# Performance work log

Hardware: AMD Instinct MI355X
Metric: run time of the kernel (lower is better)

## Reference

```python
import jax, jax.numpy as jnp
import numpy as np

T, H = 2048, 2048          # tokens, hidden_size
E, I = 16, 768             # num_experts, moe_intermediate_size
K = 2                      # top_k


def setup_inputs() -> dict:
    key = jax.random.key(0)
    k1, k2, k3, k4, k5 = jax.random.split(key, 5)
    hidden_states = jax.random.normal(k1, (T, H), dtype=jnp.float32)
    top_k_index = jax.random.randint(k2, (T, K), 0, E, dtype=jnp.int64)
    top_k_weights = jax.random.uniform(k3, (T, K), dtype=jnp.float32)
    gate_up_proj = jax.random.normal(k4, (E, 2 * I, H), dtype=jnp.float32) * 0.02
    down_proj = jax.random.normal(k5, (E, H, I), dtype=jnp.float32) * 0.02
    return {
        "hidden_states": hidden_states,
        "top_k_index": top_k_index,
        "top_k_weights": top_k_weights,
        "gate_up_proj": gate_up_proj,
        "down_proj": down_proj,
    }


def reference(hidden_states, top_k_index, top_k_weights, gate_up_proj, down_proj):
    # Dense combine-weight matrix C[t, e] = sum of routing weights of token t for expert e.
    # Scatter-add matches index_add_ semantics (duplicate expert picks sum their weights,
    # which equals the eager per-(token, k) accumulation since the expert FFN is the same).
    t_idx = jnp.arange(hidden_states.shape[0])[:, None]
    C = jnp.zeros((hidden_states.shape[0], gate_up_proj.shape[0]), dtype=hidden_states.dtype)
    C = C.at[t_idx, top_k_index].add(top_k_weights.astype(hidden_states.dtype))

    inter = down_proj.shape[2]
    # [T, E, 2I]: each expert's gate_up GEMM applied to every token (zero-weight tokens
    # contribute nothing after combining with C).
    gu = jnp.einsum("th,eoh->teo", hidden_states, gate_up_proj)
    gate, up = gu[..., :inter], gu[..., inter:]
    h = jax.nn.silu(gate) * up                      # [T, E, I]
    y = jnp.einsum("tei,ehi->teh", h, down_proj)    # [T, E, H]
    return jnp.einsum("teh,te->th", y, C)           # weighted combine -> [T, H]
```

## Files before the change

kernel.cpp:

```cpp
#include <hip/hip_runtime.h>
#include <hip/hip_bf16.h>
#include <cstdint>
#include <cstddef>

#define T_TOK 2048
#define HID   2048
#define NEXP  16
#define INTER 768
#define TOPK  2
#define CAP   1024
#define MBLK  8

using short8  = __attribute__((ext_vector_type(8))) short;
using f32x16  = __attribute__((ext_vector_type(16))) float;

#define MFMA(a,b,c) __builtin_amdgcn_mfma_f32_32x32x16_bf16((a),(b),(c),0,0,0)

__device__ inline ushort bf16h(float x) {
    union { __hip_bfloat16 b; ushort u; } cv; cv.b = __float2bfloat16(x); return cv.u;
}
__device__ inline void gl16(const void* g, void* l) {
    __builtin_amdgcn_global_load_lds((const __attribute__((address_space(1))) void*)g,
                                     (__attribute__((address_space(3))) void*)l, 16, 0, 0);
}
__device__ inline void split8(float4 a, float4 b, short8& h, short8& l) {
    float v[8] = {a.x,a.y,a.z,a.w,b.x,b.y,b.z,b.w};
    #pragma unroll
    for (int j = 0; j < 8; ++j) {
        ushort hb = bf16h(v[j]);
        float hf = __uint_as_float(((uint32_t)hb) << 16);
        h[j] = (short)hb;
        l[j] = (short)bf16h(v[j] - hf);
    }
}

__global__ __launch_bounds__(256)
void route_kernel(const int* __restrict__ idx, const float* __restrict__ wts,
                  int* __restrict__ counts, int* __restrict__ pair_tk,
                  float* __restrict__ pair_w) {
    int p = blockIdx.x * blockDim.x + threadIdx.x;
    if (p >= T_TOK * TOPK) return;
    int e = idx[p];
    int pos = atomicAdd(&counts[e], 1);
    if (pos < CAP) {
        pair_tk[e * CAP + pos] = p;
        pair_w [e * CAP + pos] = wts[p];
    }
}

__global__ __launch_bounds__(256)
void prep_bf16_kernel(const float4* __restrict__ src, ushort4* __restrict__ dst, int n4) {
    int stride = gridDim.x * blockDim.x;
    for (int i = blockIdx.x*blockDim.x + threadIdx.x; i < n4; i += stride) {
        float4 v = src[i];
        dst[i] = make_ushort4(bf16h(v.x), bf16h(v.y), bf16h(v.z), bf16h(v.w));
    }
}

__global__ __launch_bounds__(256)
void prep_hilo_kernel(const float4* __restrict__ src, ushort4* __restrict__ hi,
                      ushort4* __restrict__ lo, int n4) {
    int stride = gridDim.x * blockDim.x;
    for (int i = blockIdx.x*blockDim.x + threadIdx.x; i < n4; i += stride) {
        float4 v = src[i];
        ushort h0=bf16h(v.x), h1=bf16h(v.y), h2=bf16h(v.z), h3=bf16h(v.w);
        hi[i] = make_ushort4(h0,h1,h2,h3);
        lo[i] = make_ushort4(bf16h(v.x - __uint_as_float((uint32_t)h0<<16)),
                             bf16h(v.y - __uint_as_float((uint32_t)h1<<16)),
                             bf16h(v.z - __uint_as_float((uint32_t)h2<<16)),
                             bf16h(v.w - __uint_as_float((uint32_t)h3<<16)));
    }
}

__global__ __launch_bounds__(256, 3)
void s1mm_kernel(const ushort* __restrict__ hshi, const ushort* __restrict__ hslo,
                 const ushort* __restrict__ gupb,
                 const int* __restrict__ counts, const int* __restrict__ pair_tk,
                 float* __restrict__ gu) {
    __shared__ ushort Ab[2][8*512];
    __shared__ ushort Bb[2][16*512];
    __shared__ int s_tk[64];

    const int lin  = blockIdx.x;
    const int work = (lin & 7)*192 + (lin >> 3);
    const int x = work % 6, y = (work/6) & 7, z = work/48;
    const int e = z >> 1, ks = z & 1;
    const int cnt = min(counts[e], CAP);
    const int m0 = y*64;
    if (m0 >= cnt) return;
    const int n0 = x*128;

    const int tid = threadIdx.x, ln = tid & 63, w = tid >> 6;
    if (tid < 64) s_tk[tid] = pair_tk[e*CAP + min(m0+tid, cnt-1)];
    __syncthreads();

    const int lr = ln & 31, oc = (ln >> 5)*8;
    const int tkA = s_tk[(w & 1)*32 + lr];
    const ushort* hp = (w >> 1) ? hslo : hshi;
    const ushort* aA = hp + (size_t)(tkA >> 1)*HID + ks*1024 + oc;
    const ushort* bG = gupb + ((size_t)e*(2*INTER) + (n0 + w*32 + lr))*HID + ks*1024 + oc;
    const ushort* bU = gupb + ((size_t)e*(2*INTER) + (INTER + n0 + w*32 + lr))*HID + ks*1024 + oc;

    f32x16 accg[2], accu[2];
    #pragma unroll
    for (int i=0;i<16;++i){accg[0][i]=0.f;accg[1][i]=0.f;accu[0][i]=0.f;accu[1][i]=0.f;}

#define S1_STAGE(buf, k32) { const int kb=(k32)*32;            \
    gl16(aA+kb,    &Ab[buf][(2*w+0)*512]);                     \
    gl16(aA+kb+16, &Ab[buf][(2*w+1)*512]);                     \
    gl16(bG+kb,    &Bb[buf][(2*w+0)*512]);                     \
    gl16(bG+kb+16, &Bb[buf][(2*w+1)*512]);                     \
    gl16(bU+kb,    &Bb[buf][(2*(4+w)+0)*512]);                 \
    gl16(bU+kb+16, &Bb[buf][(2*(4+w)+1)*512]); }

    S1_STAGE(0, 0)
    int cur = 0;
    const int ro = ln*8;
    for (int k32 = 0; k32 < 32; ++k32) {
        __syncthreads();
        if (k32 + 1 < 32) S1_STAGE(cur^1, k32+1)
        #pragma unroll
        for (int kf = 0; kf < 2; ++kf) {
            short8 ah0 = *(const short8*)&Ab[cur][(0+kf)*512 + ro];
            short8 ah1 = *(const short8*)&Ab[cur][(2+kf)*512 + ro];
            short8 al0 = *(const short8*)&Ab[cur][(4+kf)*512 + ro];
            short8 al1 = *(const short8*)&Ab[cur][(6+kf)*512 + ro];
            short8 bg  = *(const short8*)&Bb[cur][(2*w+kf)*512 + ro];
            short8 bu  = *(const short8*)&Bb[cur][(8+2*w+kf)*512 + ro];
            accg[0]=MFMA(ah0,bg,accg[0]); accg[0]=MFMA(al0,bg,accg[0]);
            accg[1]=MFMA(ah1,bg,accg[1]); accg[1]=MFMA(al1,bg,accg[1]);
            accu[0]=MFMA(ah0,bu,accu[0]); accu[0]=MFMA(al0,bu,accu[0]);
            accu[1]=MFMA(ah1,bu,accu[1]); accu[1]=MFMA(al1,bu,accu[1]);
        }
        cur ^= 1;
    }
#undef S1_STAGE

    const int crhi = (ln>>5)*4, cl = ln&31;
    const int colg = n0 + 32*w + cl;
    #pragma unroll
    for (int mi=0;mi<2;++mi)
      #pragma unroll
      for (int r=0;r<16;++r) {
        int row = mi*32 + (r&3) + 8*(r>>2) + crhi;
        if (m0 + row < cnt) {
            size_t base = (size_t)s_tk[row]*(2*INTER);
            atomicAdd(&gu[base + colg],         accg[mi][r]);
            atomicAdd(&gu[base + INTER + colg], accu[mi][r]);
        }
      }
}

__global__ __launch_bounds__(256)
void fuse_kernel(const float* __restrict__ gu, ushort* __restrict__ hhi,
                 ushort* __restrict__ hlo) {
    int id  = blockIdx.x*256 + threadIdx.x;
    int row = id / (INTER/4);
    int c4  = (id % (INTER/4)) * 4;
    const float* gr = gu + (size_t)row*(2*INTER) + c4;
    float4 g = *(const float4*)gr;
    float4 u = *(const float4*)(gr + INTER);
    float hv[4];
    hv[0] = g.x/(1.f+__expf(-g.x))*u.x;
    hv[1] = g.y/(1.f+__expf(-g.y))*u.y;
    hv[2] = g.z/(1.f+__expf(-g.z))*u.z;
    hv[3] = g.w/(1.f+__expf(-g.w))*u.w;
    ushort h0=bf16h(hv[0]), h1=bf16h(hv[1]), h2=bf16h(hv[2]), h3=bf16h(hv[3]);
    *(ushort4*)&hhi[(size_t)row*INTER + c4] = make_ushort4(h0,h1,h2,h3);
    *(ushort4*)&hlo[(size_t)row*INTER + c4] = make_ushort4(
        bf16h(hv[0]-__uint_as_float((uint32_t)h0<<16)),
        bf16h(hv[1]-__uint_as_float((uint32_t)h1<<16)),
        bf16h(hv[2]-__uint_as_float((uint32_t)h2<<16)),
        bf16h(hv[3]-__uint_as_float((uint32_t)h3<<16)));
}

__global__ __launch_bounds__(256, 3)
void s2mm_kernel(const ushort* __restrict__ h2hi, const ushort* __restrict__ h2lo,
                 const ushort* __restrict__ dwnb,
                 const int* __restrict__ counts, const int* __restrict__ pair_tk,
                 const float* __restrict__ pair_w, float* __restrict__ out) {
    __shared__ ushort Ab[2][8*512];
    __shared__ ushort Bb[2][16*512];
    __shared__ int   s_tk[64];
    __shared__ float s_w[64];

    const int lin  = blockIdx.x;
    const int work = (lin & 7)*256 + (lin >> 3);
    const int x = work & 7, y = (work >> 3) & 7, z = work >> 6;
    const int e = z >> 1, ks = z & 1;
    const int cnt = min(counts[e], CAP);
    const int m0 = y*64;
    if (m0 >= cnt) return;
    const int n0 = x*256;

    const int tid = threadIdx.x, ln = tid & 63, w = tid >> 6;
    if (tid < 64) {
        int s = min(m0+tid, cnt-1);
        s_tk[tid] = pair_tk[e*CAP + s];
        s_w[tid]  = pair_w [e*CAP + s];
    }
    __syncthreads();

    const int lr = ln & 31, oc = (ln >> 5)*8;
    const int tkA = s_tk[(w & 1)*32 + lr];
    const ushort* hp = (w >> 1) ? h2lo : h2hi;
    const ushort* aA = hp + (size_t)tkA*INTER + ks*384 + oc;
    const ushort* b0 = dwnb + ((size_t)e*HID + (n0 + (2*w+0)*32 + lr))*INTER + ks*384 + oc;
    const ushort* b1 = dwnb + ((size_t)e*HID + (n0 + (2*w+1)*32 + lr))*INTER + ks*384 + oc;

    f32x16 acc[2][2];
    #pragma unroll
    for (int mi=0;mi<2;++mi)
      #pragma unroll
      for (int ni=0;ni<2;++ni)
        #pragma unroll
        for (int i=0;i<16;++i) acc[mi][ni][i] = 0.f;

#define S2_STAGE(buf, k32) { const int kb=(k32)*32;            \
    gl16(aA+kb,    &Ab[buf][(2*w+0)*512]);                     \
    gl16(aA+kb+16, &Ab[buf][(2*w+1)*512]);                     \
    gl16(b0+kb,    &Bb[buf][(4*w+0)*512]);                     \
    gl16(b0+kb+16, &Bb[buf][(4*w+1)*512]);                     \
    gl16(b1+kb,    &Bb[buf][(4*w+2)*512]);                     \
    gl16(b1+kb+16, &Bb[buf][(4*w+3)*512]); }

    S2_STAGE(0, 0)
    int cur = 0;
    const int ro = ln*8;
    for (int k32 = 0; k32 < 12; ++k32) {
        __syncthreads();
        if (k32 + 1 < 12) S2_STAGE(cur^1, k32+1)
        #pragma unroll
        for (int kf = 0; kf < 2; ++kf) {
            short8 ah0 = *(const short8*)&Ab[cur][(0+kf)*512 + ro];
            short8 ah1 = *(const short8*)&Ab[cur][(2+kf)*512 + ro];
            short8 al0 = *(const short8*)&Ab[cur][(4+kf)*512 + ro];
            short8 al1 = *(const short8*)&Ab[cur][(6+kf)*512 + ro];
            short8 b0f = *(const short8*)&Bb[cur][(4*w+0+kf)*512 + ro];
            short8 b1f = *(const short8*)&Bb[cur][(4*w+2+kf)*512 + ro];
            acc[0][0]=MFMA(ah0,b0f,acc[0][0]); acc[0][0]=MFMA(al0,b0f,acc[0][0]);
            acc[1][0]=MFMA(ah1,b0f,acc[1][0]); acc[1][0]=MFMA(al1,b0f,acc[1][0]);
            acc[0][1]=MFMA(ah0,b1f,acc[0][1]); acc[0][1]=MFMA(al0,b1f,acc[0][1]);
            acc[1][1]=MFMA(ah1,b1f,acc[1][1]); acc[1][1]=MFMA(al1,b1f,acc[1][1]);
        }
        cur ^= 1;
    }
#undef S2_STAGE

    const int crhi = (ln>>5)*4, cl = ln&31;
    #pragma unroll
    for (int mi=0;mi<2;++mi)
      #pragma unroll
      for (int r=0;r<16;++r) {
        int row = mi*32 + (r&3) + 8*(r>>2) + crhi;
        if (m0 + row < cnt) {
            int   t  = s_tk[row] >> 1;
            float wt = s_w[row];
            #pragma unroll
            for (int ni=0;ni<2;++ni) {
                int col = n0 + 64*w + 32*ni + cl;
                atomicAdd(&out[(size_t)t*HID + col], wt*acc[mi][ni][r]);
            }
        }
      }
}

__global__ __launch_bounds__(256)
void s1_fb_kernel(const float* __restrict__ hs, const float* __restrict__ gup,
                  const int* __restrict__ counts, const int* __restrict__ pair_tk,
                  float* __restrict__ gu) {
    __shared__ ushort Ahi[4*512], Alo[4*512];
    __shared__ ushort Bhi[16*512], Blo[16*512];
    __shared__ int s_tk[64];
    const int e  = blockIdx.z >> 1;
    const int ks = blockIdx.z & 1;
    const int cnt = min(counts[e], CAP);
    const int m0  = blockIdx.y * 64;
    if (m0 >= cnt) return;
    const int n0  = blockIdx.x * 128;
    const int tid = threadIdx.x, lane = tid & 63, w = tid >> 6;
    if (tid < 64) s_tk[tid] = pair_tk[e*CAP + min(m0+tid, cnt-1)];
    __syncthreads();
    const int ar = tid & 63, aq = tid >> 6;
    const float* asrc = hs + (size_t)(s_tk[ar] >> 1)*HID + ks*1024 + aq*8;
    const int br = tid;
    const float* bsrc = gup + (size_t)e*(2*INTER)*HID
                      + (size_t)((br < 128) ? (n0+br) : (INTER + n0 + br - 128))*HID + ks*1024;
    const int fA  = (ar>>5)*2 + (aq>>1);
    const int lnA = (ar&31) + 32*(aq&1);
    const int rgB = br >> 5, lnB = br & 31;
    f32x16 accg[2], accu[2];
    #pragma unroll
    for (int i=0;i<16;++i){ accg[0][i]=0.f; accg[1][i]=0.f; accu[0][i]=0.f; accu[1][i]=0.f; }
    float4 a0c,a1c,bvc[8], a0n,a1n,bvn[8];
    a0c = *(const float4*)(asrc + 0);
    a1c = *(const float4*)(asrc + 4);
    #pragma unroll
    for (int q=0;q<8;++q) bvc[q] = *(const float4*)(bsrc + 4*q);
#define S1_BODY(A0,A1,BV,A0N,A1N,BVN,KST)                                        \
    {                                                                            \
        __syncthreads();                                                         \
        { short8 h,l; split8(A0,A1,h,l);                                         \
          *(short8*)&Ahi[(fA<<9)+(lnA<<3)] = h;                                  \
          *(short8*)&Alo[(fA<<9)+(lnA<<3)] = l; }                                \
        _Pragma("unroll")                                                        \
        for (int o=0;o<4;++o) { short8 h,l; split8(BV[2*o],BV[2*o+1],h,l);       \
          int f = rgB*2 + (o>>1); int ln2 = lnB + 32*(o&1);                      \
          *(short8*)&Bhi[(f<<9)+(ln2<<3)] = h;                                   \
          *(short8*)&Blo[(f<<9)+(ln2<<3)] = l; }                                 \
        if ((KST)+1 < 32) {                                                     \
            int ko = ((KST)+1)*32;                                              \
            A0N = *(const float4*)(asrc + ko);                                  \
            A1N = *(const float4*)(asrc + ko + 4);                              \
            _Pragma("unroll")                                                   \
            for (int q=0;q<8;++q) BVN[q] = *(const float4*)(bsrc + ko + 4*q);   \
        }                                                                       \
        __syncthreads();                                                        \
        const int ro = lane << 3;                                               \
        _Pragma("unroll")                                                       \
        for (int kf=0;kf<2;++kf) {                                              \
            short8 ah0 = *(const short8*)&Ahi[((0*2+kf)<<9)+ro];                \
            short8 ah1 = *(const short8*)&Ahi[((1*2+kf)<<9)+ro];                \
            short8 al0 = *(const short8*)&Alo[((0*2+kf)<<9)+ro];                \
            short8 al1 = *(const short8*)&Alo[((1*2+kf)<<9)+ro];                \
            short8 bgh = *(const short8*)&Bhi[(((w  )*2+kf)<<9)+ro];            \
            short8 bgl = *(const short8*)&Blo[(((w  )*2+kf)<<9)+ro];            \
            short8 buh = *(const short8*)&Bhi[(((4+w)*2+kf)<<9)+ro];            \
            short8 bul = *(const short8*)&Blo[(((4+w)*2+kf)<<9)+ro];            \
            accg[0] = MFMA(ah0,bgh,accg[0]);                                    \
            accg[1] = MFMA(ah1,bgh,accg[1]);                                    \
            accu[0] = MFMA(ah0,buh,accu[0]);                                    \
            accu[1] = MFMA(ah1,buh,accu[1]);                                    \
            accg[0] = MFMA(al0,bgh,accg[0]);                                    \
            accg[1] = MFMA(al1,bgh,accg[1]);                                    \
            accu[0] = MFMA(al0,buh,accu[0]);                                    \
            accu[1] = MFMA(al1,buh,accu[1]);                                    \
            accg[0] = MFMA(ah0,bgl,accg[0]);                                    \
            accg[1] = MFMA(ah1,bgl,accg[1]);                                    \
            accu[0] = MFMA(ah0,bul,accu[0]);                                    \
            accu[1] = MFMA(ah1,bul,accu[1]);                                    \
        }                                                                       \
    }
    for (int kst = 0; kst < 32; kst += 2) {
        S1_BODY(a0c,a1c,bvc,a0n,a1n,bvn,kst)
        S1_BODY(a0n,a1n,bvn,a0c,a1c,bvc,kst+1)
    }
#undef S1_BODY
    const int crhi = (lane>>5)*4, cl = lane&31;
    const int colg = n0 + 32*w + cl;
    #pragma unroll
    for (int mi=0;mi<2;++mi)
      #pragma unroll
      for (int r=0;r<16;++r) {
        int row = mi*32 + (r&3) + 8*(r>>2) + crhi;
        if (m0 + row < cnt) {
            size_t base = (size_t)s_tk[row]*(2*INTER);
            atomicAdd(&gu[base + colg],         accg[mi][r]);
            atomicAdd(&gu[base + INTER + colg], accu[mi][r]);
        }
      }
}

__global__ __launch_bounds__(256)
void s2_fb_kernel(const ushort* __restrict__ hhi, const ushort* __restrict__ hlo,
                  const float* __restrict__ dwn, const int* __restrict__ counts,
                  const int* __restrict__ pair_tk, const float* __restrict__ pair_w,
                  float* __restrict__ out) {
    __shared__ ushort Ahi[4*512], Alo[4*512];
    __shared__ ushort Bhi[16*512], Blo[16*512];
    __shared__ int   s_tk[64];
    __shared__ float s_w[64];
    const int e  = blockIdx.z >> 1;
    const int ks = blockIdx.z & 1;
    const int cnt = min(counts[e], CAP);
    const int m0  = blockIdx.y * 64;
    if (m0 >= cnt) return;
    const int n0  = blockIdx.x * 256;
    const int tid = threadIdx.x, lane = tid & 63, w = tid >> 6;
    if (tid < 64) {
        int slot = min(m0+tid, cnt-1);
        s_tk[tid] = pair_tk[e*CAP + slot];
        s_w[tid]  = pair_w [e*CAP + slot];
    }
    __syncthreads();
    const int fA = tid >> 6, lnA = tid & 63;
    const int arow = (fA>>1)*32 + (lnA & 31);
    const int aoct = lnA >> 5, akf = fA & 1;
    const size_t aoff = (size_t)s_tk[arow]*INTER + ks*384 + akf*16 + aoct*8;
    const ushort* ahsrc = hhi + aoff;
    const ushort* alsrc = hlo + aoff;
    const int br = tid;
    const float* bsrc = dwn + (size_t)e*HID*INTER + (size_t)(n0+br)*INTER + ks*384;
    const int rgB = br >> 5, lnB = br & 31;
    f32x16 acc[2][2];
    #pragma unroll
    for (int mi=0;mi<2;++mi)
      #pragma unroll
      for (int ni=0;ni<2;++ni)
        #pragma unroll
        for (int i=0;i<16;++i) acc[mi][ni][i] = 0.f;
    short8 ahc, alc, ahn, aln;
    float4 bvc[8], bvn[8];
    ahc = *(const short8*)(ahsrc);
    alc = *(const short8*)(alsrc);
    #pragma unroll
    for (int q=0;q<8;++q) bvc[q] = *(const float4*)(bsrc + 4*q);
#define S2_BODY(AH,AL,BV,AHN,ALN,BVN,KST)                                        \
    {                                                                            \
        __syncthreads();                                                         \
        *(short8*)&Ahi[(fA<<9)+(lnA<<3)] = AH;                                   \
        *(short8*)&Alo[(fA<<9)+(lnA<<3)] = AL;                                   \
        _Pragma("unroll")                                                        \
        for (int o=0;o<4;++o) { short8 h,l; split8(BV[2*o],BV[2*o+1],h,l);       \
          int f = rgB*2 + (o>>1); int ln2 = lnB + 32*(o&1);                      \
          *(short8*)&Bhi[(f<<9)+(ln2<<3)] = h;                                   \
          *(short8*)&Blo[(f<<9)+(ln2<<3)] = l; }                                 \
        if ((KST)+1 < 12) {                                                     \
            int ko = ((KST)+1)*32;                                              \
            AHN = *(const short8*)(ahsrc + ko);                                 \
            ALN = *(const short8*)(alsrc + ko);                                 \
            _Pragma("unroll")                                                   \
            for (int q=0;q<8;++q) BVN[q] = *(const float4*)(bsrc + ko + 4*q);   \
        }                                                                       \
        __syncthreads();                                                        \
        const int ro = lane << 3;                                               \
        _Pragma("unroll")                                                       \
        for (int kf=0;kf<2;++kf) {                                              \
            short8 ah0 = *(const short8*)&Ahi[((0*2+kf)<<9)+ro];                \
            short8 ah1 = *(const short8*)&Ahi[((1*2+kf)<<9)+ro];                \
            short8 al0 = *(const short8*)&Alo[((0*2+kf)<<9)+ro];                \
            short8 al1 = *(const short8*)&Alo[((1*2+kf)<<9)+ro];                \
            _Pragma("unroll")                                                   \
            for (int ni=0;ni<2;++ni) {                                          \
                short8 bh = *(const short8*)&Bhi[(((2*w+ni)*2+kf)<<9)+ro];      \
                short8 bl = *(const short8*)&Blo[(((2*w+ni)*2+kf)<<9)+ro];      \
                acc[0][ni] = MFMA(ah0,bh,acc[0][ni]);                           \
                acc[1][ni] = MFMA(ah1,bh,acc[1][ni]);                           \
                acc[0][ni] = MFMA(al0,bh,acc[0][ni]);                           \
                acc[1][ni] = MFMA(al1,bh,acc[1][ni]);                           \
                acc[0][ni] = MFMA(ah0,bl,acc[0][ni]);                           \
                acc[1][ni] = MFMA(ah1,bl,acc[1][ni]);                           \
            }                                                                   \
        }                                                                       \
    }
    for (int kst = 0; kst < 12; kst += 2) {
        S2_BODY(ahc,alc,bvc,ahn,aln,bvn,kst)
        S2_BODY(ahn,aln,bvn,ahc,alc,bvc,kst+1)
    }
#undef S2_BODY
    const int crhi = (lane>>5)*4, cl = lane&31;
    #pragma unroll
    for (int mi=0;mi<2;++mi)
      #pragma unroll
      for (int r=0;r<16;++r) {
        int row = mi*32 + (r&3) + 8*(r>>2) + crhi;
        if (m0 + row < cnt) {
            int   t  = s_tk[row] >> 1;
            float wt = s_w[row];
            #pragma unroll
            for (int ni=0;ni<2;++ni) {
                int col = n0 + 64*w + 32*ni + cl;
                atomicAdd(&out[(size_t)t*HID + col], wt*acc[mi][ni][r]);
            }
        }
      }
}

extern "C" void kernel_launch(void* const* d_in, const int* in_sizes, int n_in,
                              void* d_out, int out_size, void* d_ws, size_t ws_size,
                              hipStream_t stream) {
    const float* hs  = (const float*)d_in[0];
    const int*   idx = (const int*)  d_in[1];
    const float* wts = (const float*)d_in[2];
    const float* gup = (const float*)d_in[3];
    const float* dwn = (const float*)d_in[4];
    float* out = (float*)d_out;

    char* ws = (char*)d_ws;
    int*   counts  = (int*)ws;
    int*   pair_tk = (int*)(ws + 1024);
    float* pair_w  = (float*)(ws + 1024 + NEXP*CAP*4);

    size_t o_gu   = 262144;
    size_t o_gupb = o_gu   + (size_t)T_TOK*TOPK*2*INTER*4;
    size_t o_dwnb = o_gupb + (size_t)NEXP*2*INTER*HID*2;
    size_t o_hshi = o_dwnb + (size_t)NEXP*HID*INTER*2;
    size_t o_hslo = o_hshi + (size_t)T_TOK*HID*2;
    size_t o_h2hi = o_hslo + (size_t)T_TOK*HID*2;
    size_t o_h2lo = o_h2hi + (size_t)T_TOK*TOPK*INTER*2;
    size_t need   = o_h2lo + (size_t)T_TOK*TOPK*INTER*2;

    hipMemsetAsync(counts, 0, NEXP*sizeof(int), stream);
    hipMemsetAsync(out, 0, (size_t)T_TOK*HID*sizeof(float), stream);
    route_kernel<<<(T_TOK*TOPK + 255)/256, 256, 0, stream>>>(idx, wts, counts, pair_tk, pair_w);

    if (ws_size >= need) {
        float*  gu   = (float*)(ws + o_gu);
        ushort* gupb = (ushort*)(ws + o_gupb);
        ushort* dwnb = (ushort*)(ws + o_dwnb);
        ushort* hshi = (ushort*)(ws + o_hshi);
        ushort* hslo = (ushort*)(ws + o_hslo);
        ushort* h2hi = (ushort*)(ws + o_h2hi);
        ushort* h2lo = (ushort*)(ws + o_h2lo);

        hipMemsetAsync(gu, 0, (size_t)T_TOK*TOPK*2*INTER*4, stream);
        prep_bf16_kernel<<<2048, 256, 0, stream>>>((const float4*)gup, (ushort4*)gupb,
                                                   NEXP*2*INTER*HID/4);
        prep_bf16_kernel<<<2048, 256, 0, stream>>>((const float4*)dwn, (ushort4*)dwnb,
                                                   NEXP*HID*INTER/4);
        prep_hilo_kernel<<<1024, 256, 0, stream>>>((const float4*)hs, (ushort4*)hshi,
                                                   (ushort4*)hslo, T_TOK*HID/4);
        s1mm_kernel<<<6*MBLK*NEXP*2, 256, 0, stream>>>(hshi, hslo, gupb, counts, pair_tk, gu);
        fuse_kernel<<<(T_TOK*TOPK*INTER/4)/256, 256, 0, stream>>>(gu, h2hi, h2lo);
        s2mm_kernel<<<8*MBLK*NEXP*2, 256, 0, stream>>>(h2hi, h2lo, dwnb, counts, pair_tk,
                                                       pair_w, out);
    } else {
        float*  gu  = (float*)(ws + 262144);
        ushort* hhi = (ushort*)(ws + 262144 + 25165824);
        ushort* hlo = (ushort*)(ws + 262144 + 25165824 + 6291456);
        hipMemsetAsync(gu, 0, (size_t)T_TOK*TOPK*2*INTER*4, stream);
        s1_fb_kernel<<<dim3(INTER/128, MBLK, NEXP*2), 256, 0, stream>>>(hs, gup, counts,
                                                                        pair_tk, gu);
        fuse_kernel<<<(T_TOK*TOPK*INTER/4)/256, 256, 0, stream>>>(gu, hhi, hlo);
        s2_fb_kernel<<<dim3(HID/256, MBLK, NEXP*2), 256, 0, stream>>>(hhi, hlo, dwn, counts,
                                                                      pair_tk, pair_w, out);
    }
}
```

Measured before the change: 634.3 us.

## Pre-tile weights into MFMA fragment layout and drop atomics via split-K planes

Weight prep kernels now write bf16 gate_up and down weights directly in per-tile, per-k-step MFMA fragment order, so each GEMM stage streams contiguous blocks. The hidden-state hi/lo split is done inside s1mm from fp32 with register prefetch, removing a separate prep pass. Split-K partials go to two gu planes with plain stores and are summed in fuse, which also writes A2 pre-tiled. Stage 2 drops split-K, writes per-pair outputs to a buffer, and a combine kernel sums the two top-k slots, replacing atomics and the output memset. This assumes each token's two expert slots are distinct rows in ybuf and that no expert exceeds the capacity tiles. Workspace regions are aliased across stages, which depends on stream ordering.

```diff
diff --git a/kernel.cpp b/kernel.cpp
--- a/kernel.cpp
+++ b/kernel.cpp
@@ -10,6 +10,7 @@
 #define TOPK  2
 #define CAP   1024
 #define MBLK  8
+#define GU_PLANE 6291456
 
 using short8  = __attribute__((ext_vector_type(8))) short;
 using f32x16  = __attribute__((ext_vector_type(16))) float;
@@ -32,6 +33,12 @@
         h[j] = (short)hb;
         l[j] = (short)bf16h(v[j] - hf);
     }
+}
+__device__ inline short8 cvt8(float4 a, float4 b) {
+    short8 r;
+    r[0]=(short)bf16h(a.x); r[1]=(short)bf16h(a.y); r[2]=(short)bf16h(a.z); r[3]=(short)bf16h(a.w);
+    r[4]=(short)bf16h(b.x); r[5]=(short)bf16h(b.y); r[6]=(short)bf16h(b.z); r[7]=(short)bf16h(b.w);
+    return r;
 }
 
 __global__ __launch_bounds__(256)
@@ -49,32 +56,46 @@
 }
 
 __global__ __launch_bounds__(256)
-void prep_bf16_kernel(const float4* __restrict__ src, ushort4* __restrict__ dst, int n4) {
+void prep_s1B_kernel(const float* __restrict__ gup, ushort* __restrict__ B1) {
+    const int total = NEXP*6*64*1024;
     int stride = gridDim.x * blockDim.x;
-    for (int i = blockIdx.x*blockDim.x + threadIdx.x; i < n4; i += stride) {
-        float4 v = src[i];
-        dst[i] = make_ushort4(bf16h(v.x), bf16h(v.y), bf16h(v.z), bf16h(v.w));
-    }
-}
-
-__global__ __launch_bounds__(256)
-void prep_hilo_kernel(const float4* __restrict__ src, ushort4* __restrict__ hi,
-                      ushort4* __restrict__ lo, int n4) {
+    for (int o = blockIdx.x*blockDim.x + threadIdx.x; o < total; o += stride) {
+        int ln = o & 63, f = (o >> 6) & 15;
+        int chunk = o >> 10;
+        int k32 = chunk & 63, xe = chunk >> 6;
+        int x = xe % 6, e = xe / 6;
+        int rg = f >> 1, kf = f & 1;
+        int grow = (rg < 4) ? (x*128 + rg*32 + (ln & 31))
+                            : (768 + x*128 + (rg-4)*32 + (ln & 31));
+        int gk = k32*32 + kf*16 + (ln >> 5)*8;
+        const float* sp = gup + ((size_t)e*1536 + grow)*2048 + gk;
+        float4 a = *(const float4*)sp;
+        float4 b = *(const float4*)(sp + 4);
+        *(short8*)(B1 + (size_t)o*8) = cvt8(a, b);
+    }
+}
+
+__global__ __launch_bounds__(256)
+void prep_s2B_kernel(const float* __restrict__ dwn, ushort* __restrict__ B2) {
+    const int total = NEXP*8*24*1024;
     int stride = gridDim.x * blockDim.x;
-    for (int i = blockIdx.x*blockDim.x + threadIdx.x; i < n4; i += stride) {
-        float4 v = src[i];
-        ushort h0=bf16h(v.x), h1=bf16h(v.y), h2=bf16h(v.z), h3=bf16h(v.w);
-        hi[i] = make_ushort4(h0,h1,h2,h3);
-        lo[i] = make_ushort4(bf16h(v.x - __uint_as_float((uint32_t)h0<<16)),
-                             bf16h(v.y - __uint_as_float((uint32_t)h1<<16)),
-                             bf16h(v.z - __uint_as_float((uint32_t)h2<<16)),
-                             bf16h(v.w - __uint_as_float((uint32_t)h3<<16)));
+    for (int o = blockIdx.x*blockDim.x + threadIdx.x; o < total; o += stride) {
+        int ln = o & 63, f = (o >> 6) & 15;
+        int chunk = o >> 10;
+        int k32 = chunk % 24, xe = chunk / 24;
+        int x = xe & 7, e = xe >> 3;
+        int rg = f >> 1, kf = f & 1;
+        int grow = x*256 + rg*32 + (ln & 31);
+        int gk = k32*32 + kf*16 + (ln >> 5)*8;
+        const float* sp = dwn + ((size_t)e*2048 + grow)*768 + gk;
+        float4 a = *(const float4*)sp;
+        float4 b = *(const float4*)(sp + 4);
+        *(short8*)(B2 + (size_t)o*8) = cvt8(a, b);
     }
 }
 
 __global__ __launch_bounds__(256, 3)
-void s1mm_kernel(const ushort* __restrict__ hshi, const ushort* __restrict__ hslo,
-                 const ushort* __restrict__ gupb,
+void s1mm_kernel(const float* __restrict__ hs, const ushort* __restrict__ B1,
                  const int* __restrict__ counts, const int* __restrict__ pair_tk,
                  float* __restrict__ gu) {
     __shared__ ushort Ab[2][8*512];
@@ -88,37 +109,56 @@
     const int cnt = min(counts[e], CAP);
     const int m0 = y*64;
     if (m0 >= cnt) return;
-    const int n0 = x*128;
 
     const int tid = threadIdx.x, ln = tid & 63, w = tid >> 6;
     if (tid < 64) s_tk[tid] = pair_tk[e*CAP + min(m0+tid, cnt-1)];
     __syncthreads();
 
-    const int lr = ln & 31, oc = (ln >> 5)*8;
-    const int tkA = s_tk[(w & 1)*32 + lr];
-    const ushort* hp = (w >> 1) ? hslo : hshi;
-    const ushort* aA = hp + (size_t)(tkA >> 1)*HID + ks*1024 + oc;
-    const ushort* bG = gupb + ((size_t)e*(2*INTER) + (n0 + w*32 + lr))*HID + ks*1024 + oc;
-    const ushort* bU = gupb + ((size_t)e*(2*INTER) + (INTER + n0 + w*32 + lr))*HID + ks*1024 + oc;
+    const int s = tid >> 2, t4 = tid & 3;
+    const int rgA = s >> 5, kfA = t4 >> 1, ohA = t4 & 1;
+    const int lnA = (s & 31) + 32*ohA;
+    const int fH = rgA*2 + kfA;
+    const int fL = 4 + rgA*2 + kfA;
+    const float* asrc = hs + (size_t)(s_tk[s] >> 1)*HID + ks*1024 + t4*8;
+
+    const ushort* B1e = B1 + (size_t)(e*6 + x)*64*8192;
 
     f32x16 accg[2], accu[2];
     #pragma unroll
     for (int i=0;i<16;++i){accg[0][i]=0.f;accg[1][i]=0.f;accu[0][i]=0.f;accu[1][i]=0.f;}
 
-#define S1_STAGE(buf, k32) { const int kb=(k32)*32;            \
-    gl16(aA+kb,    &Ab[buf][(2*w+0)*512]);                     \
-    gl16(aA+kb+16, &Ab[buf][(2*w+1)*512]);                     \
-    gl16(bG+kb,    &Bb[buf][(2*w+0)*512]);                     \
-    gl16(bG+kb+16, &Bb[buf][(2*w+1)*512]);                     \
-    gl16(bU+kb,    &Bb[buf][(2*(4+w)+0)*512]);                 \
-    gl16(bU+kb+16, &Bb[buf][(2*(4+w)+1)*512]); }
-
-    S1_STAGE(0, 0)
+#define S1_STAGE_B(buf, kk) { \
+    const ushort* bc = B1e + (size_t)(ks*32 + (kk))*8192; \
+    gl16(bc + (2*w+0)*512 + ln*8, &Bb[buf][(2*w+0)*512]); \
+    gl16(bc + (2*w+1)*512 + ln*8, &Bb[buf][(2*w+1)*512]); \
+    gl16(bc + (8+2*w)*512 + ln*8, &Bb[buf][(8+2*w)*512]); \
+    gl16(bc + (9+2*w)*512 + ln*8, &Bb[buf][(9+2*w)*512]); }
+
+    {
+        float4 va = *(const float4*)(asrc);
+        float4 vb = *(const float4*)(asrc + 4);
+        S1_STAGE_B(0, 0)
+        short8 h8, l8; split8(va, vb, h8, l8);
+        *(short8*)&Ab[0][fH*512 + lnA*8] = h8;
+        *(short8*)&Ab[0][fL*512 + lnA*8] = l8;
+    }
+    float4 vaN = *(const float4*)(asrc + 32);
+    float4 vbN = *(const float4*)(asrc + 36);
+
     int cur = 0;
     const int ro = ln*8;
-    for (int k32 = 0; k32 < 32; ++k32) {
+    for (int kk = 0; kk < 32; ++kk) {
         __syncthreads();
-        if (k32 + 1 < 32) S1_STAGE(cur^1, k32+1)
+        if (kk + 1 < 32) {
+            S1_STAGE_B(cur^1, kk+1)
+            short8 h8, l8; split8(vaN, vbN, h8, l8);
+            *(short8*)&Ab[cur^1][fH*512 + lnA*8] = h8;
+            *(short8*)&Ab[cur^1][fL*512 + lnA*8] = l8;
+            if (kk + 2 < 32) {
+                vaN = *(const float4*)(asrc + (kk+2)*32);
+                vbN = *(const float4*)(asrc + (kk+2)*32 + 4);
+            }
+        }
         #pragma unroll
         for (int kf = 0; kf < 2; ++kf) {
             short8 ah0 = *(const short8*)&Ab[cur][(0+kf)*512 + ro];
@@ -134,10 +174,11 @@
         }
         cur ^= 1;
     }
-#undef S1_STAGE
-
+#undef S1_STAGE_B
+
+    float* gp = gu + (size_t)ks*GU_PLANE;
     const int crhi = (ln>>5)*4, cl = ln&31;
-    const int colg = n0 + 32*w + cl;
+    const int colg = x*128 + 32*w + cl;
     #pragma unroll
     for (int mi=0;mi<2;++mi)
       #pragma unroll
@@ -145,15 +186,163 @@
         int row = mi*32 + (r&3) + 8*(r>>2) + crhi;
         if (m0 + row < cnt) {
             size_t base = (size_t)s_tk[row]*(2*INTER);
-            atomicAdd(&gu[base + colg],         accg[mi][r]);
-            atomicAdd(&gu[base + INTER + colg], accu[mi][r]);
+            gp[base + colg]         = accg[mi][r];
+            gp[base + INTER + colg] = accu[mi][r];
         }
       }
 }
 
 __global__ __launch_bounds__(256)
-void fuse_kernel(const float* __restrict__ gu, ushort* __restrict__ hhi,
-                 ushort* __restrict__ hlo) {
+void fuse_kernel(const float* __restrict__ gu, const int* __restrict__ counts,
+                 const int* __restrict__ pair_tk, ushort* __restrict__ A2) {
+    __shared__ int s_tk[64];
+    const int tile = blockIdx.x;
+    const int e = tile >> 3, y = tile & 7;
+    const int cnt = min(counts[e], CAP);
+    const int m0 = y*64;
+    if (m0 >= cnt) return;
+    const int tid = threadIdx.x;
+    if (tid < 64) s_tk[tid] = pair_tk[e*CAP + min(m0+tid, cnt-1)];
+    __syncthreads();
+
+    const int s = tid >> 2, t4 = tid & 3;
+    const int tk = s_tk[s];
+    const float* g0 = gu + (size_t)tk*(2*INTER);
+    const float* g1 = g0 + GU_PLANE;
+    ushort* At = A2 + (size_t)tile*98304;
+    const int rg = s >> 5, kf = t4 >> 1, oh = t4 & 1;
+    const int ln2 = (s & 31) + 32*oh;
+    const int fH = rg*2 + kf, fL = 4 + rg*2 + kf;
+
+    for (int i = 0; i < 24; ++i) {
+        int ko = i*32 + t4*8;
+        float4 ga = *(const float4*)(g0 + ko);
+        float4 gb = *(const float4*)(g0 + ko + 4);
+        float4 gc = *(const float4*)(g1 + ko);
+        float4 gd = *(const float4*)(g1 + ko + 4);
+        float4 ua = *(const float4*)(g0 + INTER + ko);
+        float4 ub = *(const float4*)(g0 + INTER + ko + 4);
+        float4 uc = *(const float4*)(g1 + INTER + ko);
+        float4 ud = *(const float4*)(g1 + INTER + ko + 4);
+        float gg[8] = {ga.x+gc.x, ga.y+gc.y, ga.z+gc.z, ga.w+gc.w,
+                       gb.x+gd.x, gb.y+gd.y, gb.z+gd.z, gb.w+gd.w};
+        float uu[8] = {ua.x+uc.x, ua.y+uc.y, ua.z+uc.z, ua.w+uc.w,
+                       ub.x+ud.x, ub.y+ud.y, ub.z+ud.z, ub.w+ud.w};
+        float4 h0, h1;
+        h0.x = gg[0]/(1.f+__expf(-gg[0]))*uu[0];
+        h0.y = gg[1]/(1.f+__expf(-gg[1]))*uu[1];
+        h0.z = gg[2]/(1.f+__expf(-gg[2]))*uu[2];
+        h0.w = gg[3]/(1.f+__expf(-gg[3]))*uu[3];
+        h1.x = gg[4]/(1.f+__expf(-gg[4]))*uu[4];
+        h1.y = gg[5]/(1.f+__expf(-gg[5]))*uu[5];
+        h1.z = gg[6]/(1.f+__expf(-gg[6]))*uu[6];
+        h1.w = gg[7]/(1.f+__expf(-gg[7]))*uu[7];
+        short8 h8, l8; split8(h0, h1, h8, l8);
+        ushort* dst = At + (size_t)i*4096;
+        *(short8*)&dst[fH*512 + ln2*8] = h8;
+        *(short8*)&dst[fL*512 + ln2*8] = l8;
+    }
+}
+
+__global__ __launch_bounds__(256, 3)
+void s2mm_kernel(const ushort* __restrict__ A2, const ushort* __restrict__ B2,
+                 const int* __restrict__ counts, const int* __restrict__ pair_tk,
+                 const float* __restrict__ pair_w, float* __restrict__ ybuf) {
+    __shared__ ushort Ab[2][8*512];
+    __shared__ ushort Bb[2][16*512];
+    __shared__ int   s_tk[64];
+    __shared__ float s_w[64];
+
+    const int lin  = blockIdx.x;
+    const int work = (lin & 7)*128 + (lin >> 3);
+    const int x = work & 7, y = (work >> 3) & 7, e = work >> 6;
+    const int cnt = min(counts[e], CAP);
+    const int m0 = y*64;
+    if (m0 >= cnt) return;
+    const int n0 = x*256;
+
+    const int tid = threadIdx.x, ln = tid & 63, w = tid >> 6;
+    if (tid < 64) {
+        int sl = min(m0+tid, cnt-1);
+        s_tk[tid] = pair_tk[e*CAP + sl];
+        s_w[tid]  = pair_w [e*CAP + sl];
+    }
+    __syncthreads();
+
+    const ushort* A2t = A2 + (size_t)(e*8 + y)*98304;
+    const ushort* B2e = B2 + (size_t)(e*8 + x)*24*8192;
+
+    f32x16 acc[2][2];
+    #pragma unroll
+    for (int mi=0;mi<2;++mi)
+      #pragma unroll
+      for (int ni=0;ni<2;++ni)
+        #pragma unroll
+        for (int i=0;i<16;++i) acc[mi][ni][i] = 0.f;
+
+#define S2_STAGE(buf, k32) { \
+    const ushort* ac = A2t + (size_t)(k32)*4096; \
+    const ushort* bc = B2e + (size_t)(k32)*8192; \
+    gl16(ac + (2*w+0)*512 + ln*8, &Ab[buf][(2*w+0)*512]); \
+    gl16(ac + (2*w+1)*512 + ln*8, &Ab[buf][(2*w+1)*512]); \
+    gl16(bc + (4*w+0)*512 + ln*8, &Bb[buf][(4*w+0)*512]); \
+    gl16(bc + (4*w+1)*512 + ln*8, &Bb[buf][(4*w+1)*512]); \
+    gl16(bc + (4*w+2)*512 + ln*8, &Bb[buf][(4*w+2)*512]); \
+    gl16(bc + (4*w+3)*512 + ln*8, &Bb[buf][(4*w+3)*512]); }
+
+    S2_STAGE(0, 0)
+    int cur = 0;
+    const int ro = ln*8;
+    for (int k32 = 0; k32 < 24; ++k32) {
+        __syncthreads();
+        if (k32 + 1 < 24) S2_STAGE(cur^1, k32+1)
+        #pragma unroll
+        for (int kf = 0; kf < 2; ++kf) {
+            short8 ah0 = *(const short8*)&Ab[cur][(0+kf)*512 + ro];
+            short8 ah1 = *(const short8*)&Ab[cur][(2+kf)*512 + ro];
+            short8 al0 = *(const short8*)&Ab[cur][(4+kf)*512 + ro];
+            short8 al1 = *(const short8*)&Ab[cur][(6+kf)*512 + ro];
+            short8 b0f = *(const short8*)&Bb[cur][(4*w+0+kf)*512 + ro];
+            short8 b1f = *(const short8*)&Bb[cur][(4*w+2+kf)*512 + ro];
+            acc[0][0]=MFMA(ah0,b0f,acc[0][0]); acc[0][0]=MFMA(al0,b0f,acc[0][0]);
+            acc[1][0]=MFMA(ah1,b0f,acc[1][0]); acc[1][0]=MFMA(al1,b0f,acc[1][0]);
+            acc[0][1]=MFMA(ah0,b1f,acc[0][1]); acc[0][1]=MFMA(al0,b1f,acc[0][1]);
+            acc[1][1]=MFMA(ah1,b1f,acc[1][1]); acc[1][1]=MFMA(al1,b1f,acc[1][1]);
+        }
+        cur ^= 1;
+    }
+#undef S2_STAGE
+
+    const int crhi = (ln>>5)*4, cl = ln&31;
+    #pragma unroll
+    for (int mi=0;mi<2;++mi)
+      #pragma unroll
+      for (int r=0;r<16;++r) {
+        int row = mi*32 + (r&3) + 8*(r>>2) + crhi;
+        if (m0 + row < cnt) {
+            int   tk = s_tk[row];
+            float wt = s_w[row];
+            #pragma unroll
+            for (int ni=0;ni<2;++ni) {
+                int col = n0 + 64*w + 32*ni + cl;
+                ybuf[(size_t)tk*HID + col] = wt*acc[mi][ni][r];
+            }
+        }
+      }
+}
+
+__global__ __launch_bounds__(256)
+void combine_kernel(const float4* __restrict__ ybuf, float4* __restrict__ out) {
+    int id = blockIdx.x*256 + threadIdx.x;
+    int t = id >> 9, c = id & 511;
+    float4 a = ybuf[(size_t)(2*t)*512 + c];
+    float4 b = ybuf[(size_t)(2*t+1)*512 + c];
+    out[id] = make_float4(a.x+b.x, a.y+b.y, a.z+b.z, a.w+b.w);
+}
+
+__global__ __launch_bounds__(256)
+void fuse_fb_kernel(const float* __restrict__ gu, ushort* __restrict__ hhi,
+                    ushort* __restrict__ hlo) {
     int id  = blockIdx.x*256 + threadIdx.x;
     int row = id / (INTER/4);
     int c4  = (id % (INTER/4)) * 4;
@@ -172,97 +361,6 @@
         bf16h(hv[1]-__uint_as_float((uint32_t)h1<<16)),
         bf16h(hv[2]-__uint_as_float((uint32_t)h2<<16)),
         bf16h(hv[3]-__uint_as_float((uint32_t)h3<<16)));
-}
-
-__global__ __launch_bounds__(256, 3)
-void s2mm_kernel(const ushort* __restrict__ h2hi, const ushort* __restrict__ h2lo,
-                 const ushort* __restrict__ dwnb,
-                 const int* __restrict__ counts, const int* __restrict__ pair_tk,
-                 const float* __restrict__ pair_w, float* __restrict__ out) {
-    __shared__ ushort Ab[2][8*512];
-    __shared__ ushort Bb[2][16*512];
-    __shared__ int   s_tk[64];
-    __shared__ float s_w[64];
-
-    const int lin  = blockIdx.x;
-    const int work = (lin & 7)*256 + (lin >> 3);
-    const int x = work & 7, y = (work >> 3) & 7, z = work >> 6;
-    const int e = z >> 1, ks = z & 1;
-    const int cnt = min(counts[e], CAP);
-    const int m0 = y*64;
-    if (m0 >= cnt) return;
-    const int n0 = x*256;
-
-    const int tid = threadIdx.x, ln = tid & 63, w = tid >> 6;
-    if (tid < 64) {
-        int s = min(m0+tid, cnt-1);
-        s_tk[tid] = pair_tk[e*CAP + s];
-        s_w[tid]  = pair_w [e*CAP + s];
-    }
-    __syncthreads();
-
-    const int lr = ln & 31, oc = (ln >> 5)*8;
-    const int tkA = s_tk[(w & 1)*32 + lr];
-    const ushort* hp = (w >> 1) ? h2lo : h2hi;
-    const ushort* aA = hp + (size_t)tkA*INTER + ks*384 + oc;
-    const ushort* b0 = dwnb + ((size_t)e*HID + (n0 + (2*w+0)*32 + lr))*INTER + ks*384 + oc;
-    const ushort* b1 = dwnb + ((size_t)e*HID + (n0 + (2*w+1)*32 + lr))*INTER + ks*384 + oc;
-
-    f32x16 acc[2][2];
-    #pragma unroll
-    for (int mi=0;mi<2;++mi)
-      #pragma unroll
-      for (int ni=0;ni<2;++ni)
-        #pragma unroll
-        for (int i=0;i<16;++i) acc[mi][ni][i] = 0.f;
-
-#define S2_STAGE(buf, k32) { const int kb=(k32)*32;            \
-    gl16(aA+kb,    &Ab[buf][(2*w+0)*512]);                     \
-    gl16(aA+kb+16, &Ab[buf][(2*w+1)*512]);                     \
-    gl16(b0+kb,    &Bb[buf][(4*w+0)*512]);                     \
-    gl16(b0+kb+16, &Bb[buf][(4*w+1)*512]);                     \
-    gl16(b1+kb,    &Bb[buf][(4*w+2)*512]);                     \
-    gl16(b1+kb+16, &Bb[buf][(4*w+3)*512]); }
-
-    S2_STAGE(0, 0)
-    int cur = 0;
-    const int ro = ln*8;
-    for (int k32 = 0; k32 < 12; ++k32) {
-        __syncthreads();
-        if (k32 + 1 < 12) S2_STAGE(cur^1, k32+1)
-        #pragma unroll
-        for (int kf = 0; kf < 2; ++kf) {
-            short8 ah0 = *(const short8*)&Ab[cur][(0+kf)*512 + ro];
-            short8 ah1 = *(const short8*)&Ab[cur][(2+kf)*512 + ro];
-            short8 al0 = *(const short8*)&Ab[cur][(4+kf)*512 + ro];
-            short8 al1 = *(const short8*)&Ab[cur][(6+kf)*512 + ro];
-            short8 b0f = *(const short8*)&Bb[cur][(4*w+0+kf)*512 + ro];
-            short8 b1f = *(const short8*)&Bb[cur][(4*w+2+kf)*512 + ro];
-            acc[0][0]=MFMA(ah0,b0f,acc[0][0]); acc[0][0]=MFMA(al0,b0f,acc[0][0]);
-            acc[1][0]=MFMA(ah1,b0f,acc[1][0]); acc[1][0]=MFMA(al1,b0f,acc[1][0]);
-            acc[0][1]=MFMA(ah0,b1f,acc[0][1]); acc[0][1]=MFMA(al0,b1f,acc[0][1]);
-            acc[1][1]=MFMA(ah1,b1f,acc[1][1]); acc[1][1]=MFMA(al1,b1f,acc[1][1]);
-        }
-        cur ^= 1;
-    }
-#undef S2_STAGE
-
-    const int crhi = (ln>>5)*4, cl = ln&31;
-    #pragma unroll
-    for (int mi=0;mi<2;++mi)
-      #pragma unroll
-      for (int r=0;r<16;++r) {
-        int row = mi*32 + (r&3) + 8*(r>>2) + crhi;
-        if (m0 + row < cnt) {
-            int   t  = s_tk[row] >> 1;
-            float wt = s_w[row];
-            #pragma unroll
-            for (int ni=0;ni<2;++ni) {
-                int col = n0 + 64*w + 32*ni + cl;
-                atomicAdd(&out[(size_t)t*HID + col], wt*acc[mi][ni][r]);
-            }
-        }
-      }
 }
 
 __global__ __launch_bounds__(256)
@@ -481,47 +579,35 @@
     int*   pair_tk = (int*)(ws + 1024);
     float* pair_w  = (float*)(ws + 1024 + NEXP*CAP*4);
 
-    size_t o_gu   = 262144;
-    size_t o_gupb = o_gu   + (size_t)T_TOK*TOPK*2*INTER*4;
-    size_t o_dwnb = o_gupb + (size_t)NEXP*2*INTER*HID*2;
-    size_t o_hshi = o_dwnb + (size_t)NEXP*HID*INTER*2;
-    size_t o_hslo = o_hshi + (size_t)T_TOK*HID*2;
-    size_t o_h2hi = o_hslo + (size_t)T_TOK*HID*2;
-    size_t o_h2lo = o_h2hi + (size_t)T_TOK*TOPK*INTER*2;
-    size_t need   = o_h2lo + (size_t)T_TOK*TOPK*INTER*2;
+    size_t o_gu  = 262144;
+    size_t o_B1  = o_gu + 50331648;
+    size_t need  = o_B1 + 100663296;
 
     hipMemsetAsync(counts, 0, NEXP*sizeof(int), stream);
-    hipMemsetAsync(out, 0, (size_t)T_TOK*HID*sizeof(float), stream);
     route_kernel<<<(T_TOK*TOPK + 255)/256, 256, 0, stream>>>(idx, wts, counts, pair_tk, pair_w);
 
     if (ws_size >= need) {
         float*  gu   = (float*)(ws + o_gu);
-        ushort* gupb = (ushort*)(ws + o_gupb);
-        ushort* dwnb = (ushort*)(ws + o_dwnb);
-        ushort* hshi = (ushort*)(ws + o_hshi);
-        ushort* hslo = (ushort*)(ws + o_hslo);
-        ushort* h2hi = (ushort*)(ws + o_h2hi);
-        ushort* h2lo = (ushort*)(ws + o_h2lo);
-
-        hipMemsetAsync(gu, 0, (size_t)T_TOK*TOPK*2*INTER*4, stream);
-        prep_bf16_kernel<<<2048, 256, 0, stream>>>((const float4*)gup, (ushort4*)gupb,
-                                                   NEXP*2*INTER*HID/4);
-        prep_bf16_kernel<<<2048, 256, 0, stream>>>((const float4*)dwn, (ushort4*)dwnb,
-                                                   NEXP*HID*INTER/4);
-        prep_hilo_kernel<<<1024, 256, 0, stream>>>((const float4*)hs, (ushort4*)hshi,
-                                                   (ushort4*)hslo, T_TOK*HID/4);
-        s1mm_kernel<<<6*MBLK*NEXP*2, 256, 0, stream>>>(hshi, hslo, gupb, counts, pair_tk, gu);
-        fuse_kernel<<<(T_TOK*TOPK*INTER/4)/256, 256, 0, stream>>>(gu, h2hi, h2lo);
-        s2mm_kernel<<<8*MBLK*NEXP*2, 256, 0, stream>>>(h2hi, h2lo, dwnb, counts, pair_tk,
-                                                       pair_w, out);
+        ushort* B1   = (ushort*)(ws + o_B1);
+        ushort* B2   = (ushort*)(ws + o_gu);
+        ushort* A2   = (ushort*)(ws + o_B1);
+        float*  ybuf = (float*)(ws + o_B1 + 25165824);
+
+        prep_s1B_kernel<<<4096, 256, 0, stream>>>(gup, B1);
+        s1mm_kernel<<<1536, 256, 0, stream>>>(hs, B1, counts, pair_tk, gu);
+        fuse_kernel<<<128, 256, 0, stream>>>(gu, counts, pair_tk, A2);
+        prep_s2B_kernel<<<4096, 256, 0, stream>>>(dwn, B2);
+        s2mm_kernel<<<1024, 256, 0, stream>>>(A2, B2, counts, pair_tk, pair_w, ybuf);
+        combine_kernel<<<(T_TOK*HID/4)/256, 256, 0, stream>>>((const float4*)ybuf, (float4*)out);
     } else {
         float*  gu  = (float*)(ws + 262144);
         ushort* hhi = (ushort*)(ws + 262144 + 25165824);
         ushort* hlo = (ushort*)(ws + 262144 + 25165824 + 6291456);
         hipMemsetAsync(gu, 0, (size_t)T_TOK*TOPK*2*INTER*4, stream);
+        hipMemsetAsync(out, 0, (size_t)T_TOK*HID*sizeof(float), stream);
         s1_fb_kernel<<<dim3(INTER/128, MBLK, NEXP*2), 256, 0, stream>>>(hs, gup, counts,
                                                                         pair_tk, gu);
-        fuse_kernel<<<(T_TOK*TOPK*INTER/4)/256, 256, 0, stream>>>(gu, hhi, hlo);
+        fuse_fb_kernel<<<(T_TOK*TOPK*INTER/4)/256, 256, 0, stream>>>(gu, hhi, hlo);
         s2_fb_kernel<<<dim3(HID/256, MBLK, NEXP*2), 256, 0, stream>>>(hhi, hlo, dwn, counts,
                                                                       pair_tk, pair_w, out);
     }
```

After: 576.2 us. 9.2% less time.
